# Performance work log

Measured on AMD Instinct MI355X. Metric: run time of the kernel, lower is better.

Reference implementation:

```python
import jax, jax.numpy as jnp
import numpy as np

SHAPES = ((100, 100), (50, 50), (25, 25))  # (H_l, W_l) per level
D, HEADS, HD, L, P = 256, 8, 32, 3, 4


def setup_inputs() -> dict:
    key = jax.random.key(0)
    ks = jax.random.split(key, 12)
    B = 2
    Nq = sum(h * w for h, w in SHAPES)  # 13125
    inp = {
        "query": jax.random.normal(ks[0], (B, Nq, D), jnp.float32),
        "reference_points": jax.random.uniform(ks[1], (B, Nq, L, 2), jnp.float32),
        "value0": jax.random.normal(ks[2], (B, SHAPES[0][0] * SHAPES[0][1], D), jnp.float32),
        "value1": jax.random.normal(ks[3], (B, SHAPES[1][0] * SHAPES[1][1], D), jnp.float32),
        "value2": jax.random.normal(ks[4], (B, SHAPES[2][0] * SHAPES[2][1], D), jnp.float32),
        "W_val": jax.random.normal(ks[5], (D, D), jnp.float32) * 0.05,
        "b_val": jnp.zeros((D,), jnp.float32),
        "W_off": jax.random.normal(ks[6], (D, HEADS * L * P * 2), jnp.float32) * 0.01,
        "b_off": jax.random.normal(ks[7], (HEADS * L * P * 2,), jnp.float32) * 2.0,
        "W_attn": jax.random.normal(ks[8], (D, HEADS * L * P), jnp.float32) * 0.02,
        "b_attn": jnp.zeros((HEADS * L * P,), jnp.float32),
        "W_out": jax.random.normal(ks[9], (D, D), jnp.float32) * 0.05,
        "b_out": jnp.zeros((D,), jnp.float32),
    }
    return inp


def _bilinear_sample(v, Hl, Wl, loc):
    """v: (B, heads, Hl*Wl, hd); loc: (B, Nq, heads, P, 2) normalized coords in [0,1].
    Matches torch F.grid_sample(mode='bilinear', padding_mode='zeros', align_corners=False)
    applied to grid = 2*loc - 1. Returns (B, Nq, heads, P, hd)."""
    B, heads, _, hd = v.shape
    Nq, Pn = loc.shape[1], loc.shape[3]
    # align_corners=False: pixel = ((g+1)*size - 1)/2 with g = 2*loc-1  ->  loc*size - 0.5
    x = loc[..., 0] * Wl - 0.5
    y = loc[..., 1] * Hl - 0.5
    x0 = jnp.floor(x)
    y0 = jnp.floor(y)
    wx1 = x - x0
    wy1 = y - y0
    out = jnp.zeros((B, Nq, heads, Pn, hd), v.dtype)
    for xi, wx in ((x0, 1.0 - wx1), (x0 + 1.0, wx1)):
        for yi, wy in ((y0, 1.0 - wy1), (y0 + 1.0, wy1)):
            inb = (xi >= 0) & (xi < Wl) & (yi >= 0) & (yi < Hl)
            idx = (jnp.clip(yi, 0, Hl - 1) * Wl + jnp.clip(xi, 0, Wl - 1)).astype(jnp.int32)
            idx_t = idx.transpose(0, 2, 1, 3).reshape(B, heads, Nq * Pn)  # (B,H,Nq*P)
            g = jnp.take_along_axis(v, idx_t[..., None], axis=2)  # (B,H,Nq*P,hd)
            g = g.reshape(B, heads, Nq, Pn, hd).transpose(0, 2, 1, 3, 4)
            w = (wx * wy * inb).astype(v.dtype)  # (B,Nq,heads,P)
            out = out + g * w[..., None]
    return out


def _forward(query, reference_points, values, W_val, b_val, W_off, b_off, W_attn, b_attn, W_out, b_out):
    B, Nq, _ = query.shape
    offs = (query @ W_off + b_off).reshape(B, Nq, HEADS, L, P, 2)
    attn = jax.nn.softmax((query @ W_attn + b_attn).reshape(B, Nq, HEADS, L * P), axis=-1)
    attn = attn.reshape(B, Nq, HEADS, L, P)
    out = jnp.zeros((B, Nq, HEADS, HD), query.dtype)
    for lvl, (Hl, Wl) in enumerate(SHAPES):
        # project values, split heads: (B, heads, H*W, hd)
        v = (values[lvl] @ W_val + b_val).reshape(B, Hl * Wl, HEADS, HD).transpose(0, 2, 1, 3)
        norm = jnp.array([Wl, Hl], query.dtype)
        loc = reference_points[:, :, lvl][:, :, None, None, :] + offs[:, :, :, lvl] / norm  # (B,Nq,heads,P,2)
        sampled = _bilinear_sample(v, Hl, Wl, loc)  # (B,Nq,heads,P,hd)
        out = out + jnp.einsum('bnhp,bnhpd->bnhd', attn[:, :, :, lvl], sampled)
    out = out.reshape(B, Nq, D)
    return out @ W_out + b_out  # dropout is identity at eval


def reference(query, reference_points, value0, value1, value2, W_val, b_val, W_off, b_off, W_attn, b_attn, W_out, b_out):
    return _forward(query, reference_points, (value0, value1, value2), W_val, b_val, W_off, b_off, W_attn, b_attn, W_out, b_out)
```

## Files before the change

kernel.cpp:

```cpp
#include <hip/hip_runtime.h>
#include <hip/hip_bf16.h>
#include <math.h>

#define BATCH 2
#define NQ    13125
#define MQ    26250
#define DM    256
#define NH    8
#define HDIM  32
#define NL    3
#define NP    4
#define NTOK  13125

typedef __attribute__((ext_vector_type(8))) short bf16x8;
typedef __attribute__((ext_vector_type(8))) unsigned short u16x8;
typedef __attribute__((ext_vector_type(4))) float f32x4;

__device__ __forceinline__ short f2bf(float f) {
    unsigned u = __float_as_uint(f);
    unsigned r = (u + 0x7FFFu + ((u >> 16) & 1u)) >> 16;
    return (short)r;
}
__device__ __forceinline__ float bf2f(unsigned short u) {
    return __uint_as_float((unsigned)u << 16);
}

__device__ __forceinline__ void gld_lds16(const short* g, short* l) {
    __builtin_amdgcn_global_load_lds(
        (const __attribute__((address_space(1))) unsigned int*)g,
        (__attribute__((address_space(3))) unsigned int*)l, 16, 0, 0);
}

__global__ __launch_bounds__(256) void wprep_kernel(const float* __restrict__ Wv,
                                                    const float* __restrict__ Wo,
                                                    const float* __restrict__ Wa,
                                                    const float* __restrict__ Wu,
                                                    short* __restrict__ Wt)
{
    const int w = blockIdx.y;
    const int Ns[5]   = {256, 192, 96, 256, 96};
    const int Offs[5] = {0, 65536, 114688, 163840, 139264};
    const int N = Ns[w];
    const int flat = blockIdx.x * 256 + threadIdx.x;
    const int n = flat >> 8, k = flat & 255;
    if (n >= N) return;
    if (w == 4) { Wt[139264 + n * 256 + k] = 0; return; }
    const float* W = (w == 0) ? Wv : ((w == 1) ? Wo : ((w == 2) ? Wa : Wu));
    Wt[Offs[w] + n * 256 + k] = f2bf(W[k * N + n]);
}

__global__ __launch_bounds__(256) void cvt_kernel(const float* __restrict__ q,
                                                  const float* __restrict__ v0,
                                                  const float* __restrict__ v1,
                                                  const float* __restrict__ v2,
                                                  short* __restrict__ qb,
                                                  short* __restrict__ vcat)
{
    const int t = blockIdx.y;
    const int sz4[4] = {MQ * 64, 2 * 10000 * 64, 2 * 2500 * 64, 2 * 625 * 64};
    const int i = blockIdx.x * 256 + threadIdx.x;
    if (i >= sz4[t]) return;
    const int row = i >> 6, c = i & 63;
    const float* src = (t == 0) ? q : ((t == 1) ? v0 : ((t == 2) ? v1 : v2));
    int orow;
    short* dst;
    if (t == 0)      { orow = row;                                        dst = qb; }
    else if (t == 1) { orow = (row / 10000) * NTOK + (row % 10000);       dst = vcat; }
    else if (t == 2) { orow = (row / 2500) * NTOK + 10000 + (row % 2500); dst = vcat; }
    else             { orow = (row / 625) * NTOK + 12500 + (row % 625);   dst = vcat; }
    float4 v = ((const float4*)src)[i];
    short4 o;
    o.x = f2bf(v.x); o.y = f2bf(v.y); o.z = f2bf(v.z); o.w = f2bf(v.w);
    ((short4*)dst)[orow * 64 + c] = o;
}

template<int EPI, int NN>
__global__ __launch_bounds__(256) void gemm128(const short* __restrict__ A,
                                               const short* __restrict__ Wt,
                                               const float* __restrict__ bias0,
                                               const float* __restrict__ bias1,
                                               void* __restrict__ C0,
                                               void* __restrict__ C1)
{
    __shared__ short As[128 * 32];
    __shared__ short Bs[128 * 32];

    const int tid  = threadIdx.x;
    const int m0   = blockIdx.y * 128;
    const int n0   = blockIdx.x * 128;
    const int lane = tid & 63;
    const int wave = tid >> 6;
    const int wm   = (wave & 1) * 64;
    const int wn   = (wave >> 1) * 64;
    const int ml   = lane & 15;
    const int kq   = lane >> 4;

    const int row0 = tid >> 2;
    const int row1 = row0 + 64;
    const int kqs  = (tid & 3) ^ ((row0 >> 1) & 3);
    const short* gA0 = A  + (size_t)(m0 + row0) * 256 + kqs * 8;
    const short* gA1 = A  + (size_t)(m0 + row1) * 256 + kqs * 8;
    const short* gB0 = Wt + (size_t)(n0 + row0) * 256 + kqs * 8;
    const short* gB1 = Wt + (size_t)(n0 + row1) * 256 + kqs * 8;
    short* lA0 = As + tid * 8;
    short* lA1 = As + (256 + tid) * 8;
    short* lB0 = Bs + tid * 8;
    short* lB1 = Bs + (256 + tid) * 8;
    const bool a0ok = (m0 + row0) < MQ;
    const bool a1ok = (m0 + row1) < MQ;

    f32x4 acc[4][4] = {};

    for (int k0 = 0; k0 < 256; k0 += 32) {
        if (a0ok) gld_lds16(gA0 + k0, lA0);
        if (a1ok) gld_lds16(gA1 + k0, lA1);
        gld_lds16(gB0 + k0, lB0);
        gld_lds16(gB1 + k0, lB1);
        __syncthreads();

        bf16x8 af[4], bfr[4];
#pragma unroll
        for (int ti = 0; ti < 4; ++ti) {
            const int r = wm + ti * 16 + ml;
            af[ti] = *(const bf16x8*)&As[r * 32 + ((kq ^ ((r >> 1) & 3)) << 3)];
        }
#pragma unroll
        for (int tj = 0; tj < 4; ++tj) {
            const int r = wn + tj * 16 + ml;
            bfr[tj] = *(const bf16x8*)&Bs[r * 32 + ((kq ^ ((r >> 1) & 3)) << 3)];
        }
#pragma unroll
        for (int ti = 0; ti < 4; ++ti)
#pragma unroll
            for (int tj = 0; tj < 4; ++tj)
                acc[ti][tj] = __builtin_amdgcn_mfma_f32_16x16x32_bf16(af[ti], bfr[tj], acc[ti][tj], 0, 0, 0);

        __syncthreads();
    }

#pragma unroll
    for (int tj = 0; tj < 4; ++tj) {
        const int gn = n0 + wn + tj * 16 + ml;
#pragma unroll
        for (int ti = 0; ti < 4; ++ti) {
#pragma unroll
            for (int r = 0; r < 4; ++r) {
                const int gm = m0 + wm + ti * 16 + kq * 4 + r;
                if (gm >= MQ) continue;
                const float v = acc[ti][tj][r];
                if (EPI == 0) {
                    ((float*)C0)[(size_t)gm * NN + gn] = v + bias0[gn];
                } else if (EPI == 1) {
                    ((short*)C0)[(size_t)gm * NN + gn] = f2bf(v + bias0[gn]);
                } else {
                    if (gn < 192)      ((float*)C0)[(size_t)gm * 192 + gn]        = v + bias0[gn];
                    else if (gn < 288) ((float*)C1)[(size_t)gm * 96 + (gn - 192)] = v + bias1[gn - 192];
                }
            }
        }
    }
}

__global__ __launch_bounds__(128) void sample_kernel(const short* __restrict__ vws,
                                                     const float* __restrict__ offs,
                                                     const float* __restrict__ logits,
                                                     const float* __restrict__ refp,
                                                     short* __restrict__ mid)
{
    const int q0  = blockIdx.x * 4;
    const int tid = threadIdx.x;

    __shared__ float  s_lg[4][96];
    __shared__ float  s_ref[4][6];
    __shared__ float  s_stat[4][NH][2];
    __shared__ float4 s_w[4][96];
    __shared__ int4   s_i[4][96];

    for (int idx = tid; idx < 384; idx += 128) {
        const int qq = idx / 96, s = idx % 96;
        if (q0 + qq < MQ) s_lg[qq][s] = logits[(size_t)(q0 + qq) * 96 + s];
    }
    if (tid < 24) {
        const int qq = tid / 6, j = tid % 6;
        if (q0 + qq < MQ) s_ref[qq][j] = refp[(size_t)(q0 + qq) * 6 + j];
    }
    __syncthreads();

    if (tid < 32) {
        const int qq = tid >> 3, h = tid & 7;
        if (q0 + qq < MQ) {
            float mx = -1e30f;
#pragma unroll
            for (int i = 0; i < 12; ++i) mx = fmaxf(mx, s_lg[qq][h * 12 + i]);
            float ssum = 0.f;
#pragma unroll
            for (int i = 0; i < 12; ++i) ssum += expf(s_lg[qq][h * 12 + i] - mx);
            s_stat[qq][h][0] = mx;
            s_stat[qq][h][1] = 1.f / ssum;
        }
    }
    __syncthreads();

    for (int idx = tid; idx < 384; idx += 128) {
        const int qq = idx / 96, s = idx % 96;
        const int q  = q0 + qq;
        if (q >= MQ) continue;
        const int b  = q / NQ;
        const int h  = s / 12, i = s % 12;
        const int l  = i >> 2, p = i & 3;

        const int Hs[3] = {100, 50, 25};
        const int Wz[3] = {100, 50, 25};
        const int Lo[3] = {0, 10000, 12500};
        const int Wl = Wz[l], Hl = Hs[l];
        const float fW = (float)Wl, fH = (float)Hl;

        const float aw = expf(s_lg[qq][s] - s_stat[qq][h][0]) * s_stat[qq][h][1];

        const int oi = (((h * NL) + l) * NP + p) * 2;
        const float2 offp = *(const float2*)(offs + (size_t)q * 192 + oi);
        const float rx = s_ref[qq][l * 2 + 0];
        const float ry = s_ref[qq][l * 2 + 1];

        const float x = (rx + offp.x / fW) * fW - 0.5f;
        const float y = (ry + offp.y / fH) * fH - 0.5f;
        const float x0f = floorf(x), y0f = floorf(y);
        const int   x0 = (int)x0f,  y0 = (int)y0f;
        const float wx1 = x - x0f, wy1 = y - y0f;
        const float wx0 = 1.f - wx1, wy0 = 1.f - wy1;

        const bool xin0 = (x0 >= 0) && (x0 < Wl);
        const bool xin1 = (x0 + 1 >= 0) && (x0 + 1 < Wl);
        const bool yin0 = (y0 >= 0) && (y0 < Hl);
        const bool yin1 = (y0 + 1 >= 0) && (y0 + 1 < Hl);

        const int cx0 = min(max(x0, 0), Wl - 1);
        const int cx1 = min(max(x0 + 1, 0), Wl - 1);
        const int cy0 = min(max(y0, 0), Hl - 1);
        const int cy1 = min(max(y0 + 1, 0), Hl - 1);

        const int base = b * NTOK + Lo[l];
        int4 idxv;
        idxv.x = (base + cy0 * Wl + cx0) * 512;
        idxv.y = (base + cy0 * Wl + cx1) * 512;
        idxv.z = (base + cy1 * Wl + cx0) * 512;
        idxv.w = (base + cy1 * Wl + cx1) * 512;

        float4 w;
        w.x = (xin0 && yin0) ? aw * wx0 * wy0 : 0.f;
        w.y = (xin1 && yin0) ? aw * wx1 * wy0 : 0.f;
        w.z = (xin0 && yin1) ? aw * wx0 * wy1 : 0.f;
        w.w = (xin1 && yin1) ? aw * wx1 * wy1 : 0.f;

        s_w[qq][s] = w;
        s_i[qq][s] = idxv;
    }
    __syncthreads();

    {
        const int qq = tid >> 5;
        const int q  = q0 + qq;
        if (q < MQ) {
            const int r  = tid & 31;
            const int h  = r >> 2;
            const int c8 = (r & 3) * 8;
            const int ch = h * HDIM + c8;
            const char* vb = (const char*)vws + (size_t)ch * 2;

            float a[8] = {};
#pragma unroll
            for (int s = 0; s < 12; ++s) {
                const float4 w  = s_w[qq][h * 12 + s];
                const int4   id = s_i[qq][h * 12 + s];
                const u16x8 u0 = *(const u16x8*)(vb + id.x);
                const u16x8 u1 = *(const u16x8*)(vb + id.y);
                const u16x8 u2 = *(const u16x8*)(vb + id.z);
                const u16x8 u3 = *(const u16x8*)(vb + id.w);
#pragma unroll
                for (int j = 0; j < 8; ++j)
                    a[j] += w.x * bf2f(u0[j]) + w.y * bf2f(u1[j]) + w.z * bf2f(u2[j]) + w.w * bf2f(u3[j]);
            }
            union { u16x8 v; unsigned short s[8]; } o;
#pragma unroll
            for (int j = 0; j < 8; ++j) o.s[j] = (unsigned short)f2bf(a[j]);
            *(u16x8*)(mid + (size_t)q * DM + ch) = o.v;
        }
    }
}

extern "C" void kernel_launch(void* const* d_in, const int* in_sizes, int n_in,
                              void* d_out, int out_size, void* d_ws, size_t ws_size,
                              hipStream_t stream)
{
    const float* query  = (const float*)d_in[0];
    const float* refp   = (const float*)d_in[1];
    const float* v0     = (const float*)d_in[2];
    const float* v1     = (const float*)d_in[3];
    const float* v2     = (const float*)d_in[4];
    const float* W_val  = (const float*)d_in[5];
    const float* b_val  = (const float*)d_in[6];
    const float* W_off  = (const float*)d_in[7];
    const float* b_off  = (const float*)d_in[8];
    const float* W_attn = (const float*)d_in[9];
    const float* b_attn = (const float*)d_in[10];
    const float* W_out  = (const float*)d_in[11];
    const float* b_out  = (const float*)d_in[12];
    float* out = (float*)d_out;

    float* ws   = (float*)d_ws;
    float* offs = ws;
    float* lgts = offs + (size_t)MQ * 192;
    short* vws  = (short*)(lgts + (size_t)MQ * 96);
    short* mid  = vws + (size_t)MQ * DM;
    short* qbf  = mid + (size_t)MQ * DM;
    short* vcat = qbf + (size_t)MQ * DM;
    short* Wt   = vcat + (size_t)MQ * DM;
    short* Wt_val = Wt;
    short* Wt_off = Wt + 65536;
    short* Wt_out = Wt + 163840;

    {
        dim3 grid(256, 5);
        wprep_kernel<<<grid, 256, 0, stream>>>(W_val, W_off, W_attn, W_out, Wt);
    }
    {
        dim3 grid((MQ * 64 + 255) / 256, 4);
        cvt_kernel<<<grid, 256, 0, stream>>>(query, v0, v1, v2, qbf, vcat);
    }
    {
        dim3 grid(2, (MQ + 127) / 128);
        gemm128<1, 256><<<grid, 256, 0, stream>>>(vcat, Wt_val, b_val, nullptr, vws, nullptr);
    }
    {
        dim3 grid(3, (MQ + 127) / 128);
        gemm128<2, 384><<<grid, 256, 0, stream>>>(qbf, Wt_off, b_off, b_attn, offs, lgts);
    }
    sample_kernel<<<(MQ + 3) / 4, 128, 0, stream>>>(vws, offs, lgts, refp, mid);
    {
        dim3 grid(2, (MQ + 127) / 128);
        gemm128<0, 256><<<grid, 256, 0, stream>>>(mid, Wt_out, b_out, nullptr, out, nullptr);
    }
}
```

Baseline: 240.4 us.

## Merge value and offset GEMMs into one launch with full-K LDS A tiles

The value-projection and offset/attention GEMMs now run in one launch, selected by blockIdx.y. The GEMM core changes from a K-looped 128x128 tile to a 64-row tile whose whole 256-wide A slice is loaded into LDS once with an XOR swizzle. B fragments are read directly from global memory instead of being staged in LDS, which removes per-k-step barriers and one launch. The sampling kernel processes 8 queries per 256-thread block instead of 4 per 128. The risks are uncoalesced global B reads and 32 KB of LDS per block, which may limit occupancy.

```diff
diff --git a/kernel.cpp b/kernel.cpp
--- a/kernel.cpp
+++ b/kernel.cpp
@@ -74,119 +74,166 @@
     ((short4*)dst)[orow * 64 + c] = o;
 }
 
-template<int EPI, int NN>
-__global__ __launch_bounds__(256) void gemm128(const short* __restrict__ A,
-                                               const short* __restrict__ Wt,
-                                               const float* __restrict__ bias0,
-                                               const float* __restrict__ bias1,
-                                               void* __restrict__ C0,
-                                               void* __restrict__ C1)
-{
-    __shared__ short As[128 * 32];
-    __shared__ short Bs[128 * 32];
-
+__device__ __forceinline__ void gemm_core(const short* __restrict__ A,
+                                          const short* __restrict__ Wt,
+                                          int m0, int M, int n0,
+                                          f32x4 acc[2][4], short* As)
+{
     const int tid  = threadIdx.x;
-    const int m0   = blockIdx.y * 128;
-    const int n0   = blockIdx.x * 128;
     const int lane = tid & 63;
     const int wave = tid >> 6;
-    const int wm   = (wave & 1) * 64;
+
+#pragma unroll
+    for (int it = 0; it < 8; ++it) {
+        const int g   = it * 256 + tid;
+        const int row = g >> 5;
+        const int p   = g & 31;
+        const int c   = p ^ (row & 31);
+        if (m0 + row < M)
+            gld_lds16(A + (size_t)(m0 + row) * 256 + c * 8, As + (size_t)g * 8);
+    }
+    __syncthreads();
+
+    const int wm = (wave & 1) * 32;
+    const int wn = (wave >> 1) * 64;
+    const int ml = lane & 15;
+    const int kq = lane >> 4;
+
+#pragma unroll
+    for (int ks = 0; ks < 8; ++ks) {
+        const int cb = ks * 4;
+        bf16x8 af[2], bfr[4];
+#pragma unroll
+        for (int ti = 0; ti < 2; ++ti) {
+            const int r = wm + ti * 16 + ml;
+            const int p = (cb + kq) ^ (r & 31);
+            af[ti] = *(const bf16x8*)&As[r * 256 + p * 8];
+        }
+#pragma unroll
+        for (int tj = 0; tj < 4; ++tj) {
+            const int r = n0 + wn + tj * 16 + ml;
+            bfr[tj] = *(const bf16x8*)(Wt + (size_t)r * 256 + ks * 32 + kq * 8);
+        }
+#pragma unroll
+        for (int ti = 0; ti < 2; ++ti)
+#pragma unroll
+            for (int tj = 0; tj < 4; ++tj)
+                acc[ti][tj] = __builtin_amdgcn_mfma_f32_16x16x32_bf16(af[ti], bfr[tj], acc[ti][tj], 0, 0, 0);
+    }
+}
+
+__global__ __launch_bounds__(256) void fgemm_kernel(const short* __restrict__ vcat,
+                                                    const short* __restrict__ qbf,
+                                                    const short* __restrict__ Wt_val,
+                                                    const short* __restrict__ Wt_off,
+                                                    const float* __restrict__ b_val,
+                                                    const float* __restrict__ b_off,
+                                                    const float* __restrict__ b_attn,
+                                                    short* __restrict__ vws,
+                                                    float* __restrict__ offs,
+                                                    float* __restrict__ lgts)
+{
+    __shared__ short As[64 * 256];
+    const int y  = blockIdx.y;
+    const int m0 = blockIdx.x * 64;
+    const bool isv = (y < 2);
+    const short* A  = isv ? vcat : qbf;
+    const short* Wt = isv ? Wt_val : Wt_off;
+    const int n0 = isv ? y * 128 : (y - 2) * 128;
+
+    f32x4 acc[2][4] = {};
+    gemm_core(A, Wt, m0, MQ, n0, acc, As);
+
+    const int tid  = threadIdx.x;
+    const int lane = tid & 63;
+    const int wave = tid >> 6;
+    const int wm   = (wave & 1) * 32;
     const int wn   = (wave >> 1) * 64;
     const int ml   = lane & 15;
     const int kq   = lane >> 4;
 
-    const int row0 = tid >> 2;
-    const int row1 = row0 + 64;
-    const int kqs  = (tid & 3) ^ ((row0 >> 1) & 3);
-    const short* gA0 = A  + (size_t)(m0 + row0) * 256 + kqs * 8;
-    const short* gA1 = A  + (size_t)(m0 + row1) * 256 + kqs * 8;
-    const short* gB0 = Wt + (size_t)(n0 + row0) * 256 + kqs * 8;
-    const short* gB1 = Wt + (size_t)(n0 + row1) * 256 + kqs * 8;
-    short* lA0 = As + tid * 8;
-    short* lA1 = As + (256 + tid) * 8;
-    short* lB0 = Bs + tid * 8;
-    short* lB1 = Bs + (256 + tid) * 8;
-    const bool a0ok = (m0 + row0) < MQ;
-    const bool a1ok = (m0 + row1) < MQ;
-
-    f32x4 acc[4][4] = {};
-
-    for (int k0 = 0; k0 < 256; k0 += 32) {
-        if (a0ok) gld_lds16(gA0 + k0, lA0);
-        if (a1ok) gld_lds16(gA1 + k0, lA1);
-        gld_lds16(gB0 + k0, lB0);
-        gld_lds16(gB1 + k0, lB1);
-        __syncthreads();
-
-        bf16x8 af[4], bfr[4];
-#pragma unroll
-        for (int ti = 0; ti < 4; ++ti) {
-            const int r = wm + ti * 16 + ml;
-            af[ti] = *(const bf16x8*)&As[r * 32 + ((kq ^ ((r >> 1) & 3)) << 3)];
-        }
-#pragma unroll
-        for (int tj = 0; tj < 4; ++tj) {
-            const int r = wn + tj * 16 + ml;
-            bfr[tj] = *(const bf16x8*)&Bs[r * 32 + ((kq ^ ((r >> 1) & 3)) << 3)];
-        }
-#pragma unroll
-        for (int ti = 0; ti < 4; ++ti)
-#pragma unroll
-            for (int tj = 0; tj < 4; ++tj)
-                acc[ti][tj] = __builtin_amdgcn_mfma_f32_16x16x32_bf16(af[ti], bfr[tj], acc[ti][tj], 0, 0, 0);
-
-        __syncthreads();
-    }
-
 #pragma unroll
     for (int tj = 0; tj < 4; ++tj) {
         const int gn = n0 + wn + tj * 16 + ml;
 #pragma unroll
-        for (int ti = 0; ti < 4; ++ti) {
+        for (int ti = 0; ti < 2; ++ti) {
 #pragma unroll
             for (int r = 0; r < 4; ++r) {
                 const int gm = m0 + wm + ti * 16 + kq * 4 + r;
                 if (gm >= MQ) continue;
                 const float v = acc[ti][tj][r];
-                if (EPI == 0) {
-                    ((float*)C0)[(size_t)gm * NN + gn] = v + bias0[gn];
-                } else if (EPI == 1) {
-                    ((short*)C0)[(size_t)gm * NN + gn] = f2bf(v + bias0[gn]);
+                if (isv) {
+                    vws[(size_t)gm * 256 + gn] = f2bf(v + b_val[gn]);
                 } else {
-                    if (gn < 192)      ((float*)C0)[(size_t)gm * 192 + gn]        = v + bias0[gn];
-                    else if (gn < 288) ((float*)C1)[(size_t)gm * 96 + (gn - 192)] = v + bias1[gn - 192];
+                    if (gn < 192)      offs[(size_t)gm * 192 + gn]        = v + b_off[gn];
+                    else if (gn < 288) lgts[(size_t)gm * 96 + (gn - 192)] = v + b_attn[gn - 192];
                 }
             }
         }
     }
 }
 
-__global__ __launch_bounds__(128) void sample_kernel(const short* __restrict__ vws,
+__global__ __launch_bounds__(256) void ogemm_kernel(const short* __restrict__ A,
+                                                    const short* __restrict__ Wt,
+                                                    const float* __restrict__ bias,
+                                                    float* __restrict__ C)
+{
+    __shared__ short As[64 * 256];
+    const int m0 = blockIdx.x * 64;
+    const int n0 = blockIdx.y * 128;
+
+    f32x4 acc[2][4] = {};
+    gemm_core(A, Wt, m0, MQ, n0, acc, As);
+
+    const int tid  = threadIdx.x;
+    const int lane = tid & 63;
+    const int wave = tid >> 6;
+    const int wm   = (wave & 1) * 32;
+    const int wn   = (wave >> 1) * 64;
+    const int ml   = lane & 15;
+    const int kq   = lane >> 4;
+
+#pragma unroll
+    for (int tj = 0; tj < 4; ++tj) {
+        const int gn = n0 + wn + tj * 16 + ml;
+#pragma unroll
+        for (int ti = 0; ti < 2; ++ti) {
+#pragma unroll
+            for (int r = 0; r < 4; ++r) {
+                const int gm = m0 + wm + ti * 16 + kq * 4 + r;
+                if (gm >= MQ) continue;
+                C[(size_t)gm * 256 + gn] = acc[ti][tj][r] + bias[gn];
+            }
+        }
+    }
+}
+
+__global__ __launch_bounds__(256) void sample_kernel(const short* __restrict__ vws,
                                                      const float* __restrict__ offs,
                                                      const float* __restrict__ logits,
                                                      const float* __restrict__ refp,
                                                      short* __restrict__ mid)
 {
-    const int q0  = blockIdx.x * 4;
+    const int q0  = blockIdx.x * 8;
     const int tid = threadIdx.x;
 
-    __shared__ float  s_lg[4][96];
-    __shared__ float  s_ref[4][6];
-    __shared__ float  s_stat[4][NH][2];
-    __shared__ float4 s_w[4][96];
-    __shared__ int4   s_i[4][96];
-
-    for (int idx = tid; idx < 384; idx += 128) {
+    __shared__ float  s_lg[8][96];
+    __shared__ float  s_ref[8][6];
+    __shared__ float  s_stat[8][NH][2];
+    __shared__ float4 s_w[8][96];
+    __shared__ int4   s_i[8][96];
+
+    for (int idx = tid; idx < 768; idx += 256) {
         const int qq = idx / 96, s = idx % 96;
         if (q0 + qq < MQ) s_lg[qq][s] = logits[(size_t)(q0 + qq) * 96 + s];
     }
-    if (tid < 24) {
+    if (tid < 48) {
         const int qq = tid / 6, j = tid % 6;
         if (q0 + qq < MQ) s_ref[qq][j] = refp[(size_t)(q0 + qq) * 6 + j];
     }
     __syncthreads();
 
-    if (tid < 32) {
+    if (tid < 64) {
         const int qq = tid >> 3, h = tid & 7;
         if (q0 + qq < MQ) {
             float mx = -1e30f;
@@ -201,7 +248,7 @@
     }
     __syncthreads();
 
-    for (int idx = tid; idx < 384; idx += 128) {
+    for (int idx = tid; idx < 768; idx += 256) {
         const int qq = idx / 96, s = idx % 96;
         const int q  = q0 + qq;
         if (q >= MQ) continue;
@@ -328,16 +375,13 @@
         cvt_kernel<<<grid, 256, 0, stream>>>(query, v0, v1, v2, qbf, vcat);
     }
     {
-        dim3 grid(2, (MQ + 127) / 128);
-        gemm128<1, 256><<<grid, 256, 0, stream>>>(vcat, Wt_val, b_val, nullptr, vws, nullptr);
-    }
-    {
-        dim3 grid(3, (MQ + 127) / 128);
-        gemm128<2, 384><<<grid, 256, 0, stream>>>(qbf, Wt_off, b_off, b_attn, offs, lgts);
-    }
-    sample_kernel<<<(MQ + 3) / 4, 128, 0, stream>>>(vws, offs, lgts, refp, mid);
-    {
-        dim3 grid(2, (MQ + 127) / 128);
-        gemm128<0, 256><<<grid, 256, 0, stream>>>(mid, Wt_out, b_out, nullptr, out, nullptr);
-    }
-}
+        dim3 grid((MQ + 63) / 64, 5);
+        fgemm_kernel<<<grid, 256, 0, stream>>>(vcat, qbf, Wt_val, Wt_off,
+                                               b_val, b_off, b_attn, vws, offs, lgts);
+    }
+    sample_kernel<<<(MQ + 7) / 8, 256, 0, stream>>>(vws, offs, lgts, refp, mid);
+    {
+        dim3 grid((MQ + 63) / 64, 2);
+        ogemm_kernel<<<grid, 256, 0, stream>>>(mid, Wt_out, b_out, out);
+    }
+}
```

Measured after the change: 264.5 us. +10.0%, slower.

## Merge prep kernels and input GEMMs, widen sampler to 256 threads

Applied to the files above, without the earlier changes.

The weight transpose and the activation bf16 conversion now run in a single launch, and the value-projection and offset/logit GEMMs share one grid, cutting launches and letting the two GEMMs overlap on the device. The sampling kernel now uses 256 threads per 4 queries, each doing 4 channels with 8-byte loads instead of 8 channels with 16-byte loads. This raises parallelism in the gather at the cost of narrower memory transactions and more index arithmetic per byte.

```diff
diff --git a/kernel.cpp b/kernel.cpp
--- a/kernel.cpp
+++ b/kernel.cpp
@@ -13,7 +13,6 @@
 #define NTOK  13125
 
 typedef __attribute__((ext_vector_type(8))) short bf16x8;
-typedef __attribute__((ext_vector_type(8))) unsigned short u16x8;
 typedef __attribute__((ext_vector_type(4))) float f32x4;
 
 __device__ __forceinline__ short f2bf(float f) {
@@ -31,63 +30,60 @@
         (__attribute__((address_space(3))) unsigned int*)l, 16, 0, 0);
 }
 
-__global__ __launch_bounds__(256) void wprep_kernel(const float* __restrict__ Wv,
-                                                    const float* __restrict__ Wo,
-                                                    const float* __restrict__ Wa,
-                                                    const float* __restrict__ Wu,
-                                                    short* __restrict__ Wt)
-{
-    const int w = blockIdx.y;
-    const int Ns[5]   = {256, 192, 96, 256, 96};
-    const int Offs[5] = {0, 65536, 114688, 163840, 139264};
-    const int N = Ns[w];
-    const int flat = blockIdx.x * 256 + threadIdx.x;
-    const int n = flat >> 8, k = flat & 255;
-    if (n >= N) return;
-    if (w == 4) { Wt[139264 + n * 256 + k] = 0; return; }
-    const float* W = (w == 0) ? Wv : ((w == 1) ? Wo : ((w == 2) ? Wa : Wu));
-    Wt[Offs[w] + n * 256 + k] = f2bf(W[k * N + n]);
-}
-
-__global__ __launch_bounds__(256) void cvt_kernel(const float* __restrict__ q,
-                                                  const float* __restrict__ v0,
-                                                  const float* __restrict__ v1,
-                                                  const float* __restrict__ v2,
-                                                  short* __restrict__ qb,
-                                                  short* __restrict__ vcat)
-{
-    const int t = blockIdx.y;
-    const int sz4[4] = {MQ * 64, 2 * 10000 * 64, 2 * 2500 * 64, 2 * 625 * 64};
-    const int i = blockIdx.x * 256 + threadIdx.x;
-    if (i >= sz4[t]) return;
-    const int row = i >> 6, c = i & 63;
-    const float* src = (t == 0) ? q : ((t == 1) ? v0 : ((t == 2) ? v1 : v2));
-    int orow;
-    short* dst;
-    if (t == 0)      { orow = row;                                        dst = qb; }
-    else if (t == 1) { orow = (row / 10000) * NTOK + (row % 10000);       dst = vcat; }
-    else if (t == 2) { orow = (row / 2500) * NTOK + 10000 + (row % 2500); dst = vcat; }
-    else             { orow = (row / 625) * NTOK + 12500 + (row % 625);   dst = vcat; }
-    float4 v = ((const float4*)src)[i];
-    short4 o;
-    o.x = f2bf(v.x); o.y = f2bf(v.y); o.z = f2bf(v.z); o.w = f2bf(v.w);
-    ((short4*)dst)[orow * 64 + c] = o;
-}
-
-template<int EPI, int NN>
-__global__ __launch_bounds__(256) void gemm128(const short* __restrict__ A,
-                                               const short* __restrict__ Wt,
-                                               const float* __restrict__ bias0,
-                                               const float* __restrict__ bias1,
-                                               void* __restrict__ C0,
-                                               void* __restrict__ C1)
-{
-    __shared__ short As[128 * 32];
-    __shared__ short Bs[128 * 32];
-
+__global__ __launch_bounds__(256) void prep_kernel(const float* __restrict__ Wv,
+                                                   const float* __restrict__ Wo,
+                                                   const float* __restrict__ Wa,
+                                                   const float* __restrict__ Wu,
+                                                   const float* __restrict__ q,
+                                                   const float* __restrict__ v0,
+                                                   const float* __restrict__ v1,
+                                                   const float* __restrict__ v2,
+                                                   short* __restrict__ Wt,
+                                                   short* __restrict__ qb,
+                                                   short* __restrict__ vcat)
+{
+    const int bid = blockIdx.x;
+    const int tid = threadIdx.x;
+    if (bid < 1280) {
+        const int w  = bid >> 8;
+        const int Ns[5]   = {256, 192, 96, 256, 96};
+        const int Offs[5] = {0, 65536, 114688, 163840, 139264};
+        const int N = Ns[w];
+        const int flat = (bid & 255) * 256 + tid;
+        const int n = flat >> 8, k = flat & 255;
+        if (n >= N) return;
+        if (w == 4) { Wt[139264 + n * 256 + k] = 0; return; }
+        const float* W = (w == 0) ? Wv : ((w == 1) ? Wo : ((w == 2) ? Wa : Wu));
+        Wt[Offs[w] + n * 256 + k] = f2bf(W[k * N + n]);
+    } else {
+        const int i_flat = (bid - 1280) * 256 + tid;
+        int i, t;
+        if (i_flat < 1680000)      { t = 0; i = i_flat; }
+        else if (i_flat < 2960000) { t = 1; i = i_flat - 1680000; }
+        else if (i_flat < 3280000) { t = 2; i = i_flat - 2960000; }
+        else                       { t = 3; i = i_flat - 3280000; }
+        const int row = i >> 6, c = i & 63;
+        const float* src = (t == 0) ? q : ((t == 1) ? v0 : ((t == 2) ? v1 : v2));
+        int orow;
+        short* dst;
+        if (t == 0)      { orow = row;                                        dst = qb; }
+        else if (t == 1) { orow = (row / 10000) * NTOK + (row % 10000);       dst = vcat; }
+        else if (t == 2) { orow = (row / 2500) * NTOK + 10000 + (row % 2500); dst = vcat; }
+        else             { orow = (row / 625) * NTOK + 12500 + (row % 625);   dst = vcat; }
+        float4 v = ((const float4*)src)[i];
+        short4 o;
+        o.x = f2bf(v.x); o.y = f2bf(v.y); o.z = f2bf(v.z); o.w = f2bf(v.w);
+        ((short4*)dst)[orow * 64 + c] = o;
+    }
+}
+
+__device__ __forceinline__ void gemm_core128(const short* __restrict__ A,
+                                             const short* __restrict__ Wt,
+                                             int m0, int n0,
+                                             f32x4 (&acc)[4][4],
+                                             short* As, short* Bs)
+{
     const int tid  = threadIdx.x;
-    const int m0   = blockIdx.y * 128;
-    const int n0   = blockIdx.x * 128;
     const int lane = tid & 63;
     const int wave = tid >> 6;
     const int wm   = (wave & 1) * 64;
@@ -109,8 +105,6 @@
     const bool a0ok = (m0 + row0) < MQ;
     const bool a1ok = (m0 + row1) < MQ;
 
-    f32x4 acc[4][4] = {};
-
     for (int k0 = 0; k0 < 256; k0 += 32) {
         if (a0ok) gld_lds16(gA0 + k0, lA0);
         if (a1ok) gld_lds16(gA1 + k0, lA1);
@@ -137,6 +131,39 @@
 
         __syncthreads();
     }
+}
+
+__global__ __launch_bounds__(256) void gemm5_kernel(const short* __restrict__ vcat,
+                                                    const short* __restrict__ qbf,
+                                                    const short* __restrict__ Wt_val,
+                                                    const short* __restrict__ Wt_off,
+                                                    const float* __restrict__ b_val,
+                                                    const float* __restrict__ b_off,
+                                                    const float* __restrict__ b_attn,
+                                                    short* __restrict__ vws,
+                                                    float* __restrict__ offs,
+                                                    float* __restrict__ lgts)
+{
+    __shared__ short As[128 * 32];
+    __shared__ short Bs[128 * 32];
+
+    const int y   = blockIdx.y;
+    const int m0  = blockIdx.x * 128;
+    const bool isv = (y < 2);
+    const short* A  = isv ? vcat : qbf;
+    const short* Wt = isv ? Wt_val : Wt_off;
+    const int n0 = isv ? y * 128 : (y - 2) * 128;
+
+    f32x4 acc[4][4] = {};
+    gemm_core128(A, Wt, m0, n0, acc, As, Bs);
+
+    const int tid  = threadIdx.x;
+    const int lane = tid & 63;
+    const int wave = tid >> 6;
+    const int wm   = (wave & 1) * 64;
+    const int wn   = (wave >> 1) * 64;
+    const int ml   = lane & 15;
+    const int kq   = lane >> 4;
 
 #pragma unroll
     for (int tj = 0; tj < 4; ++tj) {
@@ -148,20 +175,54 @@
                 const int gm = m0 + wm + ti * 16 + kq * 4 + r;
                 if (gm >= MQ) continue;
                 const float v = acc[ti][tj][r];
-                if (EPI == 0) {
-                    ((float*)C0)[(size_t)gm * NN + gn] = v + bias0[gn];
-                } else if (EPI == 1) {
-                    ((short*)C0)[(size_t)gm * NN + gn] = f2bf(v + bias0[gn]);
+                if (isv) {
+                    vws[(size_t)gm * 256 + gn] = f2bf(v + b_val[gn]);
                 } else {
-                    if (gn < 192)      ((float*)C0)[(size_t)gm * 192 + gn]        = v + bias0[gn];
-                    else if (gn < 288) ((float*)C1)[(size_t)gm * 96 + (gn - 192)] = v + bias1[gn - 192];
+                    if (gn < 192)      offs[(size_t)gm * 192 + gn]        = v + b_off[gn];
+                    else if (gn < 288) lgts[(size_t)gm * 96 + (gn - 192)] = v + b_attn[gn - 192];
                 }
             }
         }
     }
 }
 
-__global__ __launch_bounds__(128) void sample_kernel(const short* __restrict__ vws,
+__global__ __launch_bounds__(256) void ogemm_kernel(const short* __restrict__ A,
+                                                    const short* __restrict__ Wt,
+                                                    const float* __restrict__ bias,
+                                                    float* __restrict__ C)
+{
+    __shared__ short As[128 * 32];
+    __shared__ short Bs[128 * 32];
+    const int m0 = blockIdx.y * 128;
+    const int n0 = blockIdx.x * 128;
+
+    f32x4 acc[4][4] = {};
+    gemm_core128(A, Wt, m0, n0, acc, As, Bs);
+
+    const int tid  = threadIdx.x;
+    const int lane = tid & 63;
+    const int wave = tid >> 6;
+    const int wm   = (wave & 1) * 64;
+    const int wn   = (wave >> 1) * 64;
+    const int ml   = lane & 15;
+    const int kq   = lane >> 4;
+
+#pragma unroll
+    for (int tj = 0; tj < 4; ++tj) {
+        const int gn = n0 + wn + tj * 16 + ml;
+#pragma unroll
+        for (int ti = 0; ti < 4; ++ti) {
+#pragma unroll
+            for (int r = 0; r < 4; ++r) {
+                const int gm = m0 + wm + ti * 16 + kq * 4 + r;
+                if (gm >= MQ) continue;
+                C[(size_t)gm * 256 + gn] = acc[ti][tj][r] + bias[gn];
+            }
+        }
+    }
+}
+
+__global__ __launch_bounds__(256) void sample_kernel(const short* __restrict__ vws,
                                                      const float* __restrict__ offs,
                                                      const float* __restrict__ logits,
                                                      const float* __restrict__ refp,
@@ -176,13 +237,15 @@
     __shared__ float4 s_w[4][96];
     __shared__ int4   s_i[4][96];
 
-    for (int idx = tid; idx < 384; idx += 128) {
+    for (int idx = tid; idx < 384; idx += 256) {
         const int qq = idx / 96, s = idx % 96;
-        if (q0 + qq < MQ) s_lg[qq][s] = logits[(size_t)(q0 + qq) * 96 + s];
+        const int q = q0 + qq;
+        if (q < MQ) s_lg[qq][s] = logits[(size_t)q * 96 + s];
     }
     if (tid < 24) {
         const int qq = tid / 6, j = tid % 6;
-        if (q0 + qq < MQ) s_ref[qq][j] = refp[(size_t)(q0 + qq) * 6 + j];
+        const int q = q0 + qq;
+        if (q < MQ) s_ref[qq][j] = refp[(size_t)q * 6 + j];
     }
     __syncthreads();
 
@@ -201,7 +264,7 @@
     }
     __syncthreads();
 
-    for (int idx = tid; idx < 384; idx += 128) {
+    for (int idx = tid; idx < 384; idx += 256) {
         const int qq = idx / 96, s = idx % 96;
         const int q  = q0 + qq;
         if (q >= MQ) continue;
@@ -241,10 +304,10 @@
 
         const int base = b * NTOK + Lo[l];
         int4 idxv;
-        idxv.x = (base + cy0 * Wl + cx0) * 512;
-        idxv.y = (base + cy0 * Wl + cx1) * 512;
-        idxv.z = (base + cy1 * Wl + cx0) * 512;
-        idxv.w = (base + cy1 * Wl + cx1) * 512;
+        idxv.x = base + cy0 * Wl + cx0;
+        idxv.y = base + cy0 * Wl + cx1;
+        idxv.z = base + cy1 * Wl + cx0;
+        idxv.w = base + cy1 * Wl + cx1;
 
         float4 w;
         w.x = (xin0 && yin0) ? aw * wx0 * wy0 : 0.f;
@@ -258,32 +321,31 @@
     __syncthreads();
 
     {
-        const int qq = tid >> 5;
+        const int qq = tid >> 6;
         const int q  = q0 + qq;
         if (q < MQ) {
-            const int r  = tid & 31;
-            const int h  = r >> 2;
-            const int c8 = (r & 3) * 8;
-            const int ch = h * HDIM + c8;
-            const char* vb = (const char*)vws + (size_t)ch * 2;
-
-            float a[8] = {};
+            const int r  = tid & 63;
+            const int h  = r >> 3;
+            const int c4 = (r & 7) * 4;
+            const int ch = h * HDIM + c4;
+
+            float a0 = 0.f, a1 = 0.f, a2 = 0.f, a3 = 0.f;
 #pragma unroll
             for (int s = 0; s < 12; ++s) {
                 const float4 w  = s_w[qq][h * 12 + s];
                 const int4   id = s_i[qq][h * 12 + s];
-                const u16x8 u0 = *(const u16x8*)(vb + id.x);
-                const u16x8 u1 = *(const u16x8*)(vb + id.y);
-                const u16x8 u2 = *(const u16x8*)(vb + id.z);
-                const u16x8 u3 = *(const u16x8*)(vb + id.w);
-#pragma unroll
-                for (int j = 0; j < 8; ++j)
-                    a[j] += w.x * bf2f(u0[j]) + w.y * bf2f(u1[j]) + w.z * bf2f(u2[j]) + w.w * bf2f(u3[j]);
+                const ushort4 u0 = *(const ushort4*)(vws + (size_t)id.x * DM + ch);
+                const ushort4 u1 = *(const ushort4*)(vws + (size_t)id.y * DM + ch);
+                const ushort4 u2 = *(const ushort4*)(vws + (size_t)id.z * DM + ch);
+                const ushort4 u3 = *(const ushort4*)(vws + (size_t)id.w * DM + ch);
+                a0 += w.x * bf2f(u0.x) + w.y * bf2f(u1.x) + w.z * bf2f(u2.x) + w.w * bf2f(u3.x);
+                a1 += w.x * bf2f(u0.y) + w.y * bf2f(u1.y) + w.z * bf2f(u2.y) + w.w * bf2f(u3.y);
+                a2 += w.x * bf2f(u0.z) + w.y * bf2f(u1.z) + w.z * bf2f(u2.z) + w.w * bf2f(u3.z);
+                a3 += w.x * bf2f(u0.w) + w.y * bf2f(u1.w) + w.z * bf2f(u2.w) + w.w * bf2f(u3.w);
             }
-            union { u16x8 v; unsigned short s[8]; } o;
-#pragma unroll
-            for (int j = 0; j < 8; ++j) o.s[j] = (unsigned short)f2bf(a[j]);
-            *(u16x8*)(mid + (size_t)q * DM + ch) = o.v;
+            short4 o;
+            o.x = f2bf(a0); o.y = f2bf(a1); o.z = f2bf(a2); o.w = f2bf(a3);
+            *(short4*)(mid + (size_t)q * DM + ch) = o;
         }
     }
 }
@@ -319,25 +381,16 @@
     short* Wt_off = Wt + 65536;
     short* Wt_out = Wt + 163840;
 
+    prep_kernel<<<1280 + 13125, 256, 0, stream>>>(W_val, W_off, W_attn, W_out,
+                                                  query, v0, v1, v2, Wt, qbf, vcat);
     {
-        dim3 grid(256, 5);
-        wprep_kernel<<<grid, 256, 0, stream>>>(W_val, W_off, W_attn, W_out, Wt);
-    }
-    {
-        dim3 grid((MQ * 64 + 255) / 256, 4);
-        cvt_kernel<<<grid, 256, 0, stream>>>(query, v0, v1, v2, qbf, vcat);
-    }
+        dim3 grid((MQ + 127) / 128, 5);
+        gemm5_kernel<<<grid, 256, 0, stream>>>(vcat, qbf, Wt_val, Wt_off,
+                                               b_val, b_off, b_attn, vws, offs, lgts);
+    }
+    sample_kernel<<<(MQ + 3) / 4, 256, 0, stream>>>(vws, offs, lgts, refp, mid);
     {
         dim3 grid(2, (MQ + 127) / 128);
-        gemm128<1, 256><<<grid, 256, 0, stream>>>(vcat, Wt_val, b_val, nullptr, vws, nullptr);
-    }
-    {
-        dim3 grid(3, (MQ + 127) / 128);
-        gemm128<2, 384><<<grid, 256, 0, stream>>>(qbf, Wt_off, b_off, b_attn, offs, lgts);
-    }
-    sample_kernel<<<(MQ + 3) / 4, 128, 0, stream>>>(vws, offs, lgts, refp, mid);
-    {
-        dim3 grid(2, (MQ + 127) / 128);
-        gemm128<0, 256><<<grid, 256, 0, stream>>>(mid, Wt_out, b_out, nullptr, out, nullptr);
-    }
-}
+        ogemm_kernel<<<grid, 256, 0, stream>>>(mid, Wt_out, b_out, out);
+    }
+}
```

New measurement: 228.7 us. -4.9%, faster.
